# Kernel optimization log

Hardware: AMD Instinct MI355X
Metric: run time of the kernel (lower is better)

## Reference

```python
import jax, jax.numpy as jnp
import numpy as np

Q, L = 512, 4096


def setup_inputs() -> dict:
    key = jax.random.key(0)
    ks = jax.random.split(key, 12)
    def rn(k, shape, s=0.05):
        return jax.random.normal(k, shape, jnp.float32) * s
    return {
        "reactions": jax.random.normal(ks[0], (1, Q, 256), jnp.float32),
        "protein":   jax.random.normal(ks[1], (1, L, 1024), jnp.float32),
        # conv1d(1024->256, k=1) == pointwise linear
        "Wc":  rn(ks[2], (256, 1024)), "bc":  jnp.zeros((256,), jnp.float32),
        "W1":  rn(ks[3], (64, 256)),   "b1":  jnp.zeros((64,), jnp.float32),
        "W2":  rn(ks[4], (64, 256)),   "b2":  jnp.zeros((64,), jnp.float32),
        "Wa":  rn(ks[5], (64, 64)),    "ba":  jnp.zeros((64,), jnp.float32),
        "Wpa": rn(ks[6], (64, 64)),    "bpa": jnp.zeros((64,), jnp.float32),
        "Wra": rn(ks[7], (64, 64)),    "bra": jnp.zeros((64,), jnp.float32),
        "Wf1": rn(ks[8], (256, 128)),  "bf1": jnp.zeros((256,), jnp.float32),
        "Wf2": rn(ks[9], (128, 256)),  "bf2": jnp.zeros((128,), jnp.float32),
        "Wf3": rn(ks[10], (1, 128)),   "bf3": jnp.zeros((1,), jnp.float32),
    }


def reference(reactions, protein, Wc, bc, W1, b1, W2, b2, Wa, ba,
              Wpa, bpa, Wra, bra, Wf1, bf1, Wf2, bf2, Wf3, bf3):
    # protein: [1, L, 1024] -> 1x1 conv over channels == linear -> [L, 256]
    p = jax.nn.relu(protein[0] @ Wc.T + bc)
    # reactions: [1, Q, 256] -> [Q, 64]
    r = jax.nn.relu(reactions[0] @ W2.T + b2)
    # protein tokens -> [L, 64]
    k = jax.nn.relu(p @ W1.T + b1)

    ra = r @ Wra.T + bra            # [Q, 64]
    pa = k @ Wpa.T + bpa            # [L, 64]
    # broadcast outer-sum + relu + small linear: [Q, L, 64]
    A = jax.nn.relu(ra[:, None, :] + pa[None, :, :]) @ Wa.T + ba

    r_gate = jax.nn.sigmoid(jnp.mean(A, axis=1))   # [Q, 64]
    p_gate = jax.nn.sigmoid(jnp.mean(A, axis=0))   # [L, 64]

    rxnfp = r + r * r_gate                          # [Q, 64]
    prot = jnp.max(k + k * p_gate, axis=0)          # [64]  maxpool over L

    ctx = jnp.concatenate(
        [rxnfp, jnp.broadcast_to(prot, (rxnfp.shape[0], 64))], axis=1)  # [Q,128]

    # dropout layers are identity in eval mode
    h = jax.nn.leaky_relu(ctx @ Wf1.T + bf1)
    h = jax.nn.leaky_relu(h @ Wf2.T + bf2)
    out = h @ Wf3.T + bf3
    return out.reshape(-1)                          # [Q]
```

## Files before the change

### kernel.cpp

```cpp
#include <hip/hip_runtime.h>
#include <math.h>

#define TPB 256

typedef __attribute__((ext_vector_type(8))) short s16x8;
typedef __attribute__((ext_vector_type(4))) float f32x4;

constexpr unsigned OFF_P    = 0u;
constexpr unsigned OFF_K    = OFF_P    + 4096u*256u;
constexpr unsigned OFF_PA   = OFF_K    + 4096u*64u;
constexpr unsigned OFF_R    = OFF_PA   + 4096u*64u;
constexpr unsigned OFF_RA   = OFF_R    + 512u*64u;
constexpr unsigned OFF_SRP  = OFF_RA   + 512u*64u;
constexpr unsigned OFF_PMAX = OFF_SRP  + 8u*512u*64u;
constexpr unsigned OFF_W1T  = OFF_PMAX + 256u*64u;
constexpr unsigned OFF_W2T  = OFF_W1T  + 256u*64u;
constexpr unsigned OFF_WF1T = OFF_W2T  + 256u*64u;
constexpr unsigned OFF_WF2T = OFF_WF1T + 128u*256u;

__device__ __forceinline__ short f2bf(float x) {
  union { float f; unsigned u; } v; v.f = x;
  unsigned r = v.u + 0x7FFFu + ((v.u >> 16) & 1u);
  return (short)(r >> 16);
}

__global__ __launch_bounds__(TPB, 2) void k1_gemm(
    const float* __restrict__ prot, const float* __restrict__ Wc,
    const float* __restrict__ bc,   const float* __restrict__ W1,
    const float* __restrict__ W2,   const float* __restrict__ Wf1,
    const float* __restrict__ Wf2,  float* __restrict__ ws)
{
  int bid = blockIdx.x;
  int tid = threadIdx.x;
  if (bid >= 128) {
    int tb = bid - 128;
    if (tb < 2) {
      const float* W = (tb == 0) ? W1 : W2;
      float* WT = ws + ((tb == 0) ? OFF_W1T : OFF_W2T);
      for (int it = 0; it < 64; ++it) {
        int idx = it * TPB + tid;
        WT[idx] = W[(idx & 63) * 256 + (idx >> 6)];
      }
    } else if (tb < 4) {
      int h = tb - 2;
      for (int it = 0; it < 64; ++it) {
        int idx = h * 16384 + it * TPB + tid;
        ws[OFF_WF1T + idx] = Wf1[(idx & 255) * 128 + (idx >> 8)];
      }
    } else {
      int h = tb - 4;
      for (int it = 0; it < 64; ++it) {
        int idx = h * 16384 + it * TPB + tid;
        ws[OFF_WF2T + idx] = Wf2[(idx & 127) * 256 + (idx >> 7)];
      }
    }
    return;
  }

  __shared__ __align__(16) short Asm[64 * 72];
  __shared__ __align__(16) short Bsm[128 * 72];

  int m0 = (bid >> 1) * 64;
  int n0 = (bid & 1) * 128;
  int wave = tid >> 6, lane = tid & 63;
  int wm = (wave >> 1) * 32, wn = (wave & 1) * 64;
  int lm = lane & 15, quad = lane >> 4;

  int arow = tid >> 2, aseg = (tid & 3) * 16;
  int brow = tid >> 1, bseg = (tid & 1) * 32;

  const float* Ag = prot + (size_t)(m0 + arow) * 1024 + aseg;
  const float* Bg = Wc   + (size_t)(n0 + brow) * 1024 + bseg;

  float4 a4[4], b4[8];
#pragma unroll
  for (int i = 0; i < 4; ++i) a4[i] = *(const float4*)(Ag + i * 4);
#pragma unroll
  for (int i = 0; i < 8; ++i) b4[i] = *(const float4*)(Bg + i * 4);

  f32x4 acc[2][4] = {};

  for (int kc = 0; kc < 16; ++kc) {
    __syncthreads();
    {
      s16x8 s0, s1;
      s0[0]=f2bf(a4[0].x); s0[1]=f2bf(a4[0].y); s0[2]=f2bf(a4[0].z); s0[3]=f2bf(a4[0].w);
      s0[4]=f2bf(a4[1].x); s0[5]=f2bf(a4[1].y); s0[6]=f2bf(a4[1].z); s0[7]=f2bf(a4[1].w);
      s1[0]=f2bf(a4[2].x); s1[1]=f2bf(a4[2].y); s1[2]=f2bf(a4[2].z); s1[3]=f2bf(a4[2].w);
      s1[4]=f2bf(a4[3].x); s1[5]=f2bf(a4[3].y); s1[6]=f2bf(a4[3].z); s1[7]=f2bf(a4[3].w);
      *(s16x8*)&Asm[arow * 72 + aseg]     = s0;
      *(s16x8*)&Asm[arow * 72 + aseg + 8] = s1;
    }
#pragma unroll
    for (int h = 0; h < 4; ++h) {
      s16x8 s;
      s[0]=f2bf(b4[h*2].x);   s[1]=f2bf(b4[h*2].y);
      s[2]=f2bf(b4[h*2].z);   s[3]=f2bf(b4[h*2].w);
      s[4]=f2bf(b4[h*2+1].x); s[5]=f2bf(b4[h*2+1].y);
      s[6]=f2bf(b4[h*2+1].z); s[7]=f2bf(b4[h*2+1].w);
      *(s16x8*)&Bsm[brow * 72 + bseg + h * 8] = s;
    }
    if (kc < 15) {
#pragma unroll
      for (int i = 0; i < 4; ++i) a4[i] = *(const float4*)(Ag + (kc + 1) * 64 + i * 4);
#pragma unroll
      for (int i = 0; i < 8; ++i) b4[i] = *(const float4*)(Bg + (kc + 1) * 64 + i * 4);
    }
    __syncthreads();
#pragma unroll
    for (int ks = 0; ks < 2; ++ks) {
      s16x8 af[2], bfv[4];
#pragma unroll
      for (int mi = 0; mi < 2; ++mi)
        af[mi] = *(const s16x8*)&Asm[(wm + mi * 16 + lm) * 72 + ks * 32 + quad * 8];
#pragma unroll
      for (int ni = 0; ni < 4; ++ni)
        bfv[ni] = *(const s16x8*)&Bsm[(wn + ni * 16 + lm) * 72 + ks * 32 + quad * 8];
#pragma unroll
      for (int mi = 0; mi < 2; ++mi)
#pragma unroll
        for (int ni = 0; ni < 4; ++ni)
          acc[mi][ni] = __builtin_amdgcn_mfma_f32_16x16x32_bf16(
              af[mi], bfv[ni], acc[mi][ni], 0, 0, 0);
    }
  }

#pragma unroll
  for (int ni = 0; ni < 4; ++ni) {
    int col = n0 + wn + ni * 16 + lm;
    float bcv = bc[col];
#pragma unroll
    for (int mi = 0; mi < 2; ++mi) {
#pragma unroll
      for (int r = 0; r < 4; ++r) {
        int row = m0 + wm + mi * 16 + quad * 4 + r;
        ws[OFF_P + (unsigned)row * 256u + col] = fmaxf(acc[mi][ni][r] + bcv, 0.f);
      }
    }
  }
}

__global__ __launch_bounds__(TPB) void k2_heads(
    const float* __restrict__ reactions,
    const float* __restrict__ b1,  const float* __restrict__ b2,
    const float* __restrict__ Wpa, const float* __restrict__ bpa,
    const float* __restrict__ Wra, const float* __restrict__ bra,
    float* __restrict__ ws)
{
  __shared__ float ps[16 * 256];
  __shared__ float ks_[16 * 65];
  __shared__ float wst[64 * 65];
  int bid = blockIdx.x, tid = threadIdx.x;
  bool isProt = bid < 256;
  int row0 = (isProt ? bid : (bid - 256)) * 16;
  const float* src  = isProt ? (ws + OFF_P) : reactions;
  const float* WTg  = ws + (isProt ? OFF_W1T : OFF_W2T);
  const float* bv   = isProt ? b1 : b2;
  const float* W2nd = isProt ? Wpa : Wra;
  const float* b2nd = isProt ? bpa : bra;
  float* out1 = ws + (isProt ? OFF_K : OFF_R);
  float* out2 = ws + (isProt ? OFF_PA : OFF_RA);

#pragma unroll
  for (int it = 0; it < 4; ++it) {
    int i4 = it * TPB + tid;
    int row = i4 >> 6, c4 = (i4 & 63) * 4;
    *(float4*)&ps[row * 256 + c4] =
        *(const float4*)(src + (row0 + row) * 256u + c4);
  }
#pragma unroll
  for (int it = 0; it < 16; ++it) {
    int idx = it * TPB + tid;
    int a = idx >> 6, b = idx & 63;
    wst[b * 65 + a] = W2nd[idx];
  }
  __syncthreads();

  int j = tid & 63, g = tid >> 6;
  float acc[4];
  float bb = bv[j];
#pragma unroll
  for (int i = 0; i < 4; ++i) acc[i] = bb;
#pragma unroll 8
  for (int cc = 0; cc < 256; ++cc) {
    float w = WTg[cc * 64 + j];
#pragma unroll
    for (int i = 0; i < 4; ++i)
      acc[i] += ps[(g * 4 + i) * 256 + cc] * w;
  }
#pragma unroll
  for (int i = 0; i < 4; ++i) {
    float kv = fmaxf(acc[i], 0.f);
    int row = g * 4 + i;
    out1[(row0 + row) * 64u + j] = kv;
    ks_[row * 65 + j] = kv;
  }
  __syncthreads();

  float bb2 = b2nd[j];
  float acc2[4];
#pragma unroll
  for (int i = 0; i < 4; ++i) acc2[i] = bb2;
#pragma unroll 8
  for (int jj = 0; jj < 64; ++jj) {
    float w = wst[jj * 65 + j];
#pragma unroll
    for (int i = 0; i < 4; ++i)
      acc2[i] += ks_[(g * 4 + i) * 65 + jj] * w;
  }
#pragma unroll
  for (int i = 0; i < 4; ++i)
    out2[(row0 + g * 4 + i) * 64u + j] = acc2[i];
}

__global__ __launch_bounds__(TPB) void k3_interact(
    const float* __restrict__ Wa, const float* __restrict__ ba,
    float* __restrict__ ws)
{
  __shared__ float sm[9536];
  int bid = blockIdx.x, tid = threadIdx.x;
  int c = tid & 63, g = tid >> 6;
  const float* ra = ws + OFF_RA;
  const float* pa = ws + OFF_PA;

  if (bid < 256) {
    int qt = bid >> 3, ls = bid & 7;
    int q0 = qt * 16, l0 = ls * 512;
    float u[4], acc[4];
#pragma unroll
    for (int i = 0; i < 4; ++i) {
      u[i] = ra[(q0 + g * 4 + i) * 64u + c];
      acc[i] = 0.f;
    }
    for (int chunk = 0; chunk < 8; ++chunk) {
      unsigned base = (unsigned)(l0 + chunk * 64) * 64u;
      for (int it = 0; it < 4; ++it) {
        int i4 = it * TPB + tid;
        int row = i4 >> 4, c4 = (i4 & 15) * 4;
        *(float4*)&sm[row * 64 + c4] = *(const float4*)(pa + base + row * 64 + c4);
      }
      __syncthreads();
#pragma unroll 4
      for (int ll = 0; ll < 64; ++ll) {
        float x = sm[ll * 64 + c];
#pragma unroll
        for (int i = 0; i < 4; ++i) acc[i] += fmaxf(u[i] + x, 0.f);
      }
      __syncthreads();
    }
#pragma unroll
    for (int i = 0; i < 4; ++i)
      ws[OFF_SRP + (unsigned)(ls * 512 + q0 + g * 4 + i) * 64u + c] = acc[i];
  } else {
    int b = bid - 256;
    int l0 = b * 16;
    for (int it = 0; it < 16; ++it) {
      int idx = it * TPB + tid;
      int a = idx >> 6, bb = idx & 63;
      sm[5120 + bb * 65 + a] = Wa[idx];
    }
    float v[4], acc[4];
#pragma unroll
    for (int i = 0; i < 4; ++i) {
      v[i] = pa[(unsigned)(l0 + g * 4 + i) * 64u + c];
      acc[i] = 0.f;
    }
    for (int chunk = 0; chunk < 8; ++chunk) {
      unsigned base = (unsigned)(chunk * 64) * 64u;
      for (int it = 0; it < 4; ++it) {
        int i4 = it * TPB + tid;
        int row = i4 >> 4, c4 = (i4 & 15) * 4;
        *(float4*)&sm[row * 64 + c4] = *(const float4*)(ra + base + row * 64 + c4);
      }
      __syncthreads();
#pragma unroll 4
      for (int qq = 0; qq < 64; ++qq) {
        float x = sm[qq * 64 + c];
#pragma unroll
        for (int i = 0; i < 4; ++i) acc[i] += fmaxf(v[i] + x, 0.f);
      }
      __syncthreads();
    }
#pragma unroll
    for (int i = 0; i < 4; ++i) sm[4096 + (g * 4 + i) * 64 + c] = acc[i];
    __syncthreads();
    float vmax = 0.f;
    float bac = ba[c];
#pragma unroll
    for (int i = 0; i < 4; ++i) {
      int ll = g * 4 + i;
      float dot = 0.f;
#pragma unroll 8
      for (int jj = 0; jj < 64; ++jj)
        dot += sm[4096 + ll * 64 + jj] * sm[5120 + jj * 65 + c];
      float pg = 1.f / (1.f + __expf(-(dot * (1.f / 512.f) + bac)));
      float val = ws[OFF_K + (unsigned)(l0 + ll) * 64u + c] * (1.f + pg);
      vmax = fmaxf(vmax, val);
    }
    sm[9280 + g * 64 + c] = vmax;
    __syncthreads();
    if (tid < 64) {
      float m = fmaxf(fmaxf(sm[9280 + tid], sm[9280 + 64 + tid]),
                      fmaxf(sm[9280 + 128 + tid], sm[9280 + 192 + tid]));
      ws[OFF_PMAX + (unsigned)b * 64u + tid] = m;
    }
  }
}

__global__ __launch_bounds__(TPB) void k4_final(
    const float* __restrict__ Wa,  const float* __restrict__ ba,
    const float* __restrict__ bf1, const float* __restrict__ bf2,
    const float* __restrict__ Wf3, const float* __restrict__ bf3,
    const float* __restrict__ ws,  float* __restrict__ out)
{
  __shared__ float wa[64 * 65];
  __shared__ float mr[256];
  __shared__ float pm[256];
  __shared__ float prot[64];
  __shared__ float rx[256];
  __shared__ float h1s[4 * 256];
  __shared__ float h2s[4 * 128];
  int bid = blockIdx.x, tid = threadIdx.x;
  int q0 = bid * 4;
  int q = tid >> 6, c = tid & 63;

  for (int it = 0; it < 16; ++it) {
    int idx = it * TPB + tid;
    wa[(idx >> 6) * 65 + (idx & 63)] = Wa[idx];
  }
  {
    float s = 0.f;
#pragma unroll
    for (int ls = 0; ls < 8; ++ls)
      s += ws[OFF_SRP + (unsigned)(ls * 512 + q0 + q) * 64u + c];
    mr[q * 64 + c] = s * (1.f / 4096.f);
  }
  {
    float m = 0.f;
    for (int i = 0; i < 64; ++i)
      m = fmaxf(m, ws[OFF_PMAX + (unsigned)(q * 64 + i) * 64u + c]);
    pm[q * 64 + c] = m;
  }
  __syncthreads();
  if (tid < 64)
    prot[tid] = fmaxf(fmaxf(pm[tid], pm[64 + tid]),
                      fmaxf(pm[128 + tid], pm[192 + tid]));
  __syncthreads();
  {
    float dot = 0.f;
#pragma unroll 8
    for (int j = 0; j < 64; ++j)
      dot += mr[q * 64 + j] * wa[c * 65 + j];
    float g = 1.f / (1.f + __expf(-(dot + ba[c])));
    rx[q * 64 + c] = ws[OFF_R + (unsigned)(q0 + q) * 64u + c] * (1.f + g);
  }
  __syncthreads();
  {
    int n = tid;
    const float* wf1t = ws + OFF_WF1T;
    float a0 = 0, a1 = 0, a2 = 0, a3 = 0, c1 = 0;
#pragma unroll 4
    for (int j = 0; j < 64; ++j) {
      float w1 = wf1t[j * 256 + n];
      float w2 = wf1t[(64 + j) * 256 + n];
      c1 += prot[j] * w2;
      a0 += rx[j] * w1;
      a1 += rx[64 + j] * w1;
      a2 += rx[128 + j] * w1;
      a3 += rx[192 + j] * w1;
    }
    float bb = bf1[n] + c1;
    float v;
    v = a0 + bb; h1s[0 * 256 + n] = v > 0.f ? v : 0.01f * v;
    v = a1 + bb; h1s[1 * 256 + n] = v > 0.f ? v : 0.01f * v;
    v = a2 + bb; h1s[2 * 256 + n] = v > 0.f ? v : 0.01f * v;
    v = a3 + bb; h1s[3 * 256 + n] = v > 0.f ? v : 0.01f * v;
  }
  __syncthreads();
  {
    int m = tid & 127, qh = tid >> 7;
    const float* wf2t = ws + OFF_WF2T;
    const float* h1a = h1s + (qh * 2) * 256;
    const float* h1b = h1s + (qh * 2 + 1) * 256;
    float b0 = 0, b1 = 0;
#pragma unroll 4
    for (int j = 0; j < 256; ++j) {
      float w = wf2t[j * 128 + m];
      b0 += h1a[j] * w;
      b1 += h1b[j] * w;
    }
    float bb = bf2[m];
    float v0 = b0 + bb, v1 = b1 + bb;
    h2s[(qh * 2) * 128 + m]     = v0 > 0.f ? v0 : 0.01f * v0;
    h2s[(qh * 2 + 1) * 128 + m] = v1 > 0.f ? v1 : 0.01f * v1;
  }
  __syncthreads();
  {
    float v = h2s[q * 128 + c] * Wf3[c] + h2s[q * 128 + 64 + c] * Wf3[64 + c];
#pragma unroll
    for (int off = 32; off > 0; off >>= 1) v += __shfl_down(v, off);
    if (c == 0) out[q0 + q] = v + bf3[0];
  }
}

extern "C" void kernel_launch(void* const* d_in, const int* in_sizes, int n_in,
                              void* d_out, int out_size, void* d_ws, size_t ws_size,
                              hipStream_t stream)
{
  const float* reactions = (const float*)d_in[0];
  const float* protein   = (const float*)d_in[1];
  const float* Wc  = (const float*)d_in[2];
  const float* bc  = (const float*)d_in[3];
  const float* W1  = (const float*)d_in[4];
  const float* b1  = (const float*)d_in[5];
  const float* W2  = (const float*)d_in[6];
  const float* b2  = (const float*)d_in[7];
  const float* Wa  = (const float*)d_in[8];
  const float* ba  = (const float*)d_in[9];
  const float* Wpa = (const float*)d_in[10];
  const float* bpa = (const float*)d_in[11];
  const float* Wra = (const float*)d_in[12];
  const float* bra = (const float*)d_in[13];
  const float* Wf1 = (const float*)d_in[14];
  const float* bf1 = (const float*)d_in[15];
  const float* Wf2 = (const float*)d_in[16];
  const float* bf2 = (const float*)d_in[17];
  const float* Wf3 = (const float*)d_in[18];
  const float* bf3 = (const float*)d_in[19];
  float* ws  = (float*)d_ws;
  float* out = (float*)d_out;

  hipLaunchKernelGGL(k1_gemm, dim3(134), dim3(TPB), 0, stream,
                     protein, Wc, bc, W1, W2, Wf1, Wf2, ws);
  hipLaunchKernelGGL(k2_heads, dim3(288), dim3(TPB), 0, stream,
                     reactions, b1, b2, Wpa, bpa, Wra, bra, ws);
  hipLaunchKernelGGL(k3_interact, dim3(512), dim3(TPB), 0, stream,
                     Wa, ba, ws);
  hipLaunchKernelGGL(k4_final, dim3(128), dim3(TPB), 0, stream,
                     Wa, ba, bf1, bf2, Wf3, bf3, ws, out);
}
```

Measured before the change: 205.3 us.

## Use MFMA bf16 in head kernel, tiled weight transposes, packed bf16 conversion

The head kernel now runs both of its small projections (256->64 and 64->64) as bf16 MFMA tiles with operands staged in shared memory, instead of scalar fp32 FMAs over pre-transposed weights. As a result the W1/W2 transposes drop out of the first kernel, and the Wf1/Wf2 transposes become coalesced 32x32 shared-memory tile transposes spread across 8 blocks. Float-to-bf16 conversion uses the packed intrinsic in place of manual per-element rounding. The final kernel handles 2 queries per block across 256 blocks to spread the MLP tail over more CUs. Dropping the head projections to bf16 lowers their precision.

```diff
diff --git a/kernel.cpp b/kernel.cpp
--- a/kernel.cpp
+++ b/kernel.cpp
@@ -1,4 +1,5 @@
 #include <hip/hip_runtime.h>
+#include <hip/hip_bf16.h>
 #include <math.h>
 
 #define TPB 256
@@ -23,36 +24,48 @@
   unsigned r = v.u + 0x7FFFu + ((v.u >> 16) & 1u);
   return (short)(r >> 16);
 }
+__device__ __forceinline__ unsigned pkbf(float a, float b) {
+  __hip_bfloat162 h = __float22bfloat162_rn(make_float2(a, b));
+  union { __hip_bfloat162 h2; unsigned u; } v; v.h2 = h;
+  return v.u;
+}
+union U8 { s16x8 s; unsigned u[4]; };
 
 __global__ __launch_bounds__(TPB, 2) void k1_gemm(
     const float* __restrict__ prot, const float* __restrict__ Wc,
-    const float* __restrict__ bc,   const float* __restrict__ W1,
-    const float* __restrict__ W2,   const float* __restrict__ Wf1,
+    const float* __restrict__ bc,   const float* __restrict__ Wf1,
     const float* __restrict__ Wf2,  float* __restrict__ ws)
 {
   int bid = blockIdx.x;
   int tid = threadIdx.x;
   if (bid >= 128) {
+    __shared__ float tl[32 * 33];
     int tb = bid - 128;
-    if (tb < 2) {
-      const float* W = (tb == 0) ? W1 : W2;
-      float* WT = ws + ((tb == 0) ? OFF_W1T : OFF_W2T);
-      for (int it = 0; it < 64; ++it) {
+    for (int i = 0; i < 8; ++i) {
+      int t = tb * 8 + i;
+      const float* S; float* D; int snc, dnc, sr, sc;
+      if (t < 32) {
+        S = Wf1; D = ws + OFF_WF1T; snc = 128; dnc = 256;
+        sr = (t >> 2) * 32; sc = (t & 3) * 32;
+      } else {
+        int t2 = t - 32;
+        S = Wf2; D = ws + OFF_WF2T; snc = 256; dnc = 128;
+        sr = (t2 >> 3) * 32; sc = (t2 & 7) * 32;
+      }
+#pragma unroll
+      for (int it = 0; it < 4; ++it) {
         int idx = it * TPB + tid;
-        WT[idx] = W[(idx & 63) * 256 + (idx >> 6)];
-      }
-    } else if (tb < 4) {
-      int h = tb - 2;
-      for (int it = 0; it < 64; ++it) {
-        int idx = h * 16384 + it * TPB + tid;
-        ws[OFF_WF1T + idx] = Wf1[(idx & 255) * 128 + (idx >> 8)];
-      }
-    } else {
-      int h = tb - 4;
-      for (int it = 0; it < 64; ++it) {
-        int idx = h * 16384 + it * TPB + tid;
-        ws[OFF_WF2T + idx] = Wf2[(idx & 127) * 256 + (idx >> 7)];
-      }
+        int r = idx >> 5, c = idx & 31;
+        tl[c * 33 + r] = S[(size_t)(sr + r) * snc + sc + c];
+      }
+      __syncthreads();
+#pragma unroll
+      for (int it = 0; it < 4; ++it) {
+        int idx = it * TPB + tid;
+        int r = idx >> 5, c = idx & 31;
+        D[(size_t)(sc + r) * dnc + sr + c] = tl[r * 33 + c];
+      }
+      __syncthreads();
     }
     return;
   }
@@ -83,22 +96,22 @@
   for (int kc = 0; kc < 16; ++kc) {
     __syncthreads();
     {
-      s16x8 s0, s1;
-      s0[0]=f2bf(a4[0].x); s0[1]=f2bf(a4[0].y); s0[2]=f2bf(a4[0].z); s0[3]=f2bf(a4[0].w);
-      s0[4]=f2bf(a4[1].x); s0[5]=f2bf(a4[1].y); s0[6]=f2bf(a4[1].z); s0[7]=f2bf(a4[1].w);
-      s1[0]=f2bf(a4[2].x); s1[1]=f2bf(a4[2].y); s1[2]=f2bf(a4[2].z); s1[3]=f2bf(a4[2].w);
-      s1[4]=f2bf(a4[3].x); s1[5]=f2bf(a4[3].y); s1[6]=f2bf(a4[3].z); s1[7]=f2bf(a4[3].w);
-      *(s16x8*)&Asm[arow * 72 + aseg]     = s0;
-      *(s16x8*)&Asm[arow * 72 + aseg + 8] = s1;
+      U8 s0, s1;
+      s0.u[0] = pkbf(a4[0].x, a4[0].y); s0.u[1] = pkbf(a4[0].z, a4[0].w);
+      s0.u[2] = pkbf(a4[1].x, a4[1].y); s0.u[3] = pkbf(a4[1].z, a4[1].w);
+      s1.u[0] = pkbf(a4[2].x, a4[2].y); s1.u[1] = pkbf(a4[2].z, a4[2].w);
+      s1.u[2] = pkbf(a4[3].x, a4[3].y); s1.u[3] = pkbf(a4[3].z, a4[3].w);
+      *(s16x8*)&Asm[arow * 72 + aseg]     = s0.s;
+      *(s16x8*)&Asm[arow * 72 + aseg + 8] = s1.s;
     }
 #pragma unroll
     for (int h = 0; h < 4; ++h) {
-      s16x8 s;
-      s[0]=f2bf(b4[h*2].x);   s[1]=f2bf(b4[h*2].y);
-      s[2]=f2bf(b4[h*2].z);   s[3]=f2bf(b4[h*2].w);
-      s[4]=f2bf(b4[h*2+1].x); s[5]=f2bf(b4[h*2+1].y);
-      s[6]=f2bf(b4[h*2+1].z); s[7]=f2bf(b4[h*2+1].w);
-      *(s16x8*)&Bsm[brow * 72 + bseg + h * 8] = s;
+      U8 s;
+      s.u[0] = pkbf(b4[h*2].x,   b4[h*2].y);
+      s.u[1] = pkbf(b4[h*2].z,   b4[h*2].w);
+      s.u[2] = pkbf(b4[h*2+1].x, b4[h*2+1].y);
+      s.u[3] = pkbf(b4[h*2+1].z, b4[h*2+1].w);
+      *(s16x8*)&Bsm[brow * 72 + bseg + h * 8] = s.s;
     }
     if (kc < 15) {
 #pragma unroll
@@ -140,77 +153,121 @@
   }
 }
 
-__global__ __launch_bounds__(TPB) void k2_heads(
+__global__ __launch_bounds__(TPB, 2) void k2_heads(
     const float* __restrict__ reactions,
-    const float* __restrict__ b1,  const float* __restrict__ b2,
+    const float* __restrict__ W1,  const float* __restrict__ b1,
+    const float* __restrict__ W2,  const float* __restrict__ b2,
     const float* __restrict__ Wpa, const float* __restrict__ bpa,
     const float* __restrict__ Wra, const float* __restrict__ bra,
     float* __restrict__ ws)
 {
-  __shared__ float ps[16 * 256];
-  __shared__ float ks_[16 * 65];
-  __shared__ float wst[64 * 65];
+  __shared__ __align__(16) short Asm[32 * 264];
+  __shared__ __align__(16) short Bsm[64 * 264];
+  __shared__ __align__(16) short Ksm[32 * 72];
+  __shared__ __align__(16) short Wsm[64 * 72];
   int bid = blockIdx.x, tid = threadIdx.x;
-  bool isProt = bid < 256;
-  int row0 = (isProt ? bid : (bid - 256)) * 16;
+  bool isProt = bid < 128;
+  int row0 = (isProt ? bid : (bid - 128)) * 32;
   const float* src  = isProt ? (ws + OFF_P) : reactions;
-  const float* WTg  = ws + (isProt ? OFF_W1T : OFF_W2T);
+  const float* Wst1 = isProt ? W1 : W2;
   const float* bv   = isProt ? b1 : b2;
-  const float* W2nd = isProt ? Wpa : Wra;
+  const float* Wst2 = isProt ? Wpa : Wra;
   const float* b2nd = isProt ? bpa : bra;
   float* out1 = ws + (isProt ? OFF_K : OFF_R);
   float* out2 = ws + (isProt ? OFF_PA : OFF_RA);
 
-#pragma unroll
-  for (int it = 0; it < 4; ++it) {
-    int i4 = it * TPB + tid;
-    int row = i4 >> 6, c4 = (i4 & 63) * 4;
-    *(float4*)&ps[row * 256 + c4] =
-        *(const float4*)(src + (row0 + row) * 256u + c4);
-  }
-#pragma unroll
-  for (int it = 0; it < 16; ++it) {
-    int idx = it * TPB + tid;
-    int a = idx >> 6, b = idx & 63;
-    wst[b * 65 + a] = W2nd[idx];
-  }
-  __syncthreads();
-
-  int j = tid & 63, g = tid >> 6;
-  float acc[4];
-  float bb = bv[j];
-#pragma unroll
-  for (int i = 0; i < 4; ++i) acc[i] = bb;
-#pragma unroll 8
-  for (int cc = 0; cc < 256; ++cc) {
-    float w = WTg[cc * 64 + j];
-#pragma unroll
-    for (int i = 0; i < 4; ++i)
-      acc[i] += ps[(g * 4 + i) * 256 + cc] * w;
-  }
-#pragma unroll
-  for (int i = 0; i < 4; ++i) {
-    float kv = fmaxf(acc[i], 0.f);
-    int row = g * 4 + i;
-    out1[(row0 + row) * 64u + j] = kv;
-    ks_[row * 65 + j] = kv;
-  }
-  __syncthreads();
-
-  float bb2 = b2nd[j];
-  float acc2[4];
-#pragma unroll
-  for (int i = 0; i < 4; ++i) acc2[i] = bb2;
-#pragma unroll 8
-  for (int jj = 0; jj < 64; ++jj) {
-    float w = wst[jj * 65 + j];
-#pragma unroll
-    for (int i = 0; i < 4; ++i)
-      acc2[i] += ks_[(g * 4 + i) * 65 + jj] * w;
-  }
-#pragma unroll
-  for (int i = 0; i < 4; ++i)
-    out2[(row0 + g * 4 + i) * 64u + j] = acc2[i];
+  {
+    int row = tid >> 3, seg = (tid & 7) * 32;
+    const float* sp = src + (size_t)(row0 + row) * 256 + seg;
+    float4 f[8];
+#pragma unroll
+    for (int i = 0; i < 8; ++i) f[i] = *(const float4*)(sp + i * 4);
+#pragma unroll
+    for (int i = 0; i < 4; ++i) {
+      U8 s;
+      s.u[0] = pkbf(f[2*i].x,   f[2*i].y);
+      s.u[1] = pkbf(f[2*i].z,   f[2*i].w);
+      s.u[2] = pkbf(f[2*i+1].x, f[2*i+1].y);
+      s.u[3] = pkbf(f[2*i+1].z, f[2*i+1].w);
+      *(s16x8*)&Asm[row * 264 + seg + i * 8] = s.s;
+    }
+  }
+  {
+    int row = tid >> 2, seg = (tid & 3) * 64;
+    const float* sp = Wst1 + (size_t)row * 256 + seg;
+#pragma unroll
+    for (int i = 0; i < 8; ++i) {
+      float4 fa = *(const float4*)(sp + i * 8);
+      float4 fb = *(const float4*)(sp + i * 8 + 4);
+      U8 s;
+      s.u[0] = pkbf(fa.x, fa.y); s.u[1] = pkbf(fa.z, fa.w);
+      s.u[2] = pkbf(fb.x, fb.y); s.u[3] = pkbf(fb.z, fb.w);
+      *(s16x8*)&Bsm[row * 264 + seg + i * 8] = s.s;
+    }
+  }
+  {
+    int row = tid >> 2, seg = (tid & 3) * 16;
+    const float* sp = Wst2 + (size_t)row * 64 + seg;
+#pragma unroll
+    for (int i = 0; i < 2; ++i) {
+      float4 fa = *(const float4*)(sp + i * 8);
+      float4 fb = *(const float4*)(sp + i * 8 + 4);
+      U8 s;
+      s.u[0] = pkbf(fa.x, fa.y); s.u[1] = pkbf(fa.z, fa.w);
+      s.u[2] = pkbf(fb.x, fb.y); s.u[3] = pkbf(fb.z, fb.w);
+      *(s16x8*)&Wsm[row * 72 + seg + i * 8] = s.s;
+    }
+  }
+  __syncthreads();
+
+  int wave = tid >> 6, lane = tid & 63;
+  int lm = lane & 15, quad = lane >> 4;
+  int wm = (wave >> 1) * 16, wn = (wave & 1) * 32;
+
+  f32x4 acc[2] = {};
+#pragma unroll
+  for (int kc = 0; kc < 8; ++kc) {
+    s16x8 a = *(const s16x8*)&Asm[(wm + lm) * 264 + kc * 32 + quad * 8];
+#pragma unroll
+    for (int ni = 0; ni < 2; ++ni) {
+      s16x8 b = *(const s16x8*)&Bsm[(wn + ni * 16 + lm) * 264 + kc * 32 + quad * 8];
+      acc[ni] = __builtin_amdgcn_mfma_f32_16x16x32_bf16(a, b, acc[ni], 0, 0, 0);
+    }
+  }
+#pragma unroll
+  for (int ni = 0; ni < 2; ++ni) {
+    int col = wn + ni * 16 + lm;
+    float bb = bv[col];
+#pragma unroll
+    for (int r = 0; r < 4; ++r) {
+      int row = wm + quad * 4 + r;
+      float kv = fmaxf(acc[ni][r] + bb, 0.f);
+      out1[(size_t)(row0 + row) * 64 + col] = kv;
+      Ksm[row * 72 + col] = f2bf(kv);
+    }
+  }
+  __syncthreads();
+
+  f32x4 acc2[2] = {};
+#pragma unroll
+  for (int kc = 0; kc < 2; ++kc) {
+    s16x8 a = *(const s16x8*)&Ksm[(wm + lm) * 72 + kc * 32 + quad * 8];
+#pragma unroll
+    for (int ni = 0; ni < 2; ++ni) {
+      s16x8 b = *(const s16x8*)&Wsm[(wn + ni * 16 + lm) * 72 + kc * 32 + quad * 8];
+      acc2[ni] = __builtin_amdgcn_mfma_f32_16x16x32_bf16(a, b, acc2[ni], 0, 0, 0);
+    }
+  }
+#pragma unroll
+  for (int ni = 0; ni < 2; ++ni) {
+    int col = wn + ni * 16 + lm;
+    float bb = b2nd[col];
+#pragma unroll
+    for (int r = 0; r < 4; ++r) {
+      int row = wm + quad * 4 + r;
+      out2[(size_t)(row0 + row) * 64 + col] = acc2[ni][r] + bb;
+    }
+  }
 }
 
 __global__ __launch_bounds__(TPB) void k3_interact(
@@ -314,93 +371,91 @@
     const float* __restrict__ ws,  float* __restrict__ out)
 {
   __shared__ float wa[64 * 65];
-  __shared__ float mr[256];
+  __shared__ float mr[128];
   __shared__ float pm[256];
   __shared__ float prot[64];
-  __shared__ float rx[256];
-  __shared__ float h1s[4 * 256];
-  __shared__ float h2s[4 * 128];
+  __shared__ float rx[128];
+  __shared__ float h1s[2 * 256];
+  __shared__ float h2s[2 * 128];
+  __shared__ float red[8];
   int bid = blockIdx.x, tid = threadIdx.x;
-  int q0 = bid * 4;
-  int q = tid >> 6, c = tid & 63;
+  int q0 = bid * 2;
 
   for (int it = 0; it < 16; ++it) {
     int idx = it * TPB + tid;
     wa[(idx >> 6) * 65 + (idx & 63)] = Wa[idx];
   }
-  {
+  if (tid < 128) {
+    int q = tid >> 6, c = tid & 63;
     float s = 0.f;
 #pragma unroll
     for (int ls = 0; ls < 8; ++ls)
       s += ws[OFF_SRP + (unsigned)(ls * 512 + q0 + q) * 64u + c];
-    mr[q * 64 + c] = s * (1.f / 4096.f);
-  }
-  {
+    mr[tid] = s * (1.f / 4096.f);
+  }
+  {
+    int c = tid & 63, ch = tid >> 6;
     float m = 0.f;
+#pragma unroll 8
     for (int i = 0; i < 64; ++i)
-      m = fmaxf(m, ws[OFF_PMAX + (unsigned)(q * 64 + i) * 64u + c]);
-    pm[q * 64 + c] = m;
+      m = fmaxf(m, ws[OFF_PMAX + (unsigned)(ch * 64 + i) * 64u + c]);
+    pm[ch * 64 + c] = m;
   }
   __syncthreads();
   if (tid < 64)
     prot[tid] = fmaxf(fmaxf(pm[tid], pm[64 + tid]),
                       fmaxf(pm[128 + tid], pm[192 + tid]));
   __syncthreads();
-  {
+  if (tid < 128) {
+    int q = tid >> 6, c = tid & 63;
     float dot = 0.f;
 #pragma unroll 8
     for (int j = 0; j < 64; ++j)
       dot += mr[q * 64 + j] * wa[c * 65 + j];
     float g = 1.f / (1.f + __expf(-(dot + ba[c])));
-    rx[q * 64 + c] = ws[OFF_R + (unsigned)(q0 + q) * 64u + c] * (1.f + g);
+    rx[tid] = ws[OFF_R + (unsigned)(q0 + q) * 64u + c] * (1.f + g);
   }
   __syncthreads();
   {
     int n = tid;
     const float* wf1t = ws + OFF_WF1T;
-    float a0 = 0, a1 = 0, a2 = 0, a3 = 0, c1 = 0;
-#pragma unroll 4
+    float a0 = 0, a1 = 0, c1 = 0;
+#pragma unroll 8
     for (int j = 0; j < 64; ++j) {
       float w1 = wf1t[j * 256 + n];
       float w2 = wf1t[(64 + j) * 256 + n];
       c1 += prot[j] * w2;
       a0 += rx[j] * w1;
       a1 += rx[64 + j] * w1;
-      a2 += rx[128 + j] * w1;
-      a3 += rx[192 + j] * w1;
     }
     float bb = bf1[n] + c1;
     float v;
-    v = a0 + bb; h1s[0 * 256 + n] = v > 0.f ? v : 0.01f * v;
-    v = a1 + bb; h1s[1 * 256 + n] = v > 0.f ? v : 0.01f * v;
-    v = a2 + bb; h1s[2 * 256 + n] = v > 0.f ? v : 0.01f * v;
-    v = a3 + bb; h1s[3 * 256 + n] = v > 0.f ? v : 0.01f * v;
+    v = a0 + bb; h1s[n]       = v > 0.f ? v : 0.01f * v;
+    v = a1 + bb; h1s[256 + n] = v > 0.f ? v : 0.01f * v;
   }
   __syncthreads();
   {
     int m = tid & 127, qh = tid >> 7;
     const float* wf2t = ws + OFF_WF2T;
-    const float* h1a = h1s + (qh * 2) * 256;
-    const float* h1b = h1s + (qh * 2 + 1) * 256;
-    float b0 = 0, b1 = 0;
-#pragma unroll 4
-    for (int j = 0; j < 256; ++j) {
-      float w = wf2t[j * 128 + m];
-      b0 += h1a[j] * w;
-      b1 += h1b[j] * w;
-    }
-    float bb = bf2[m];
-    float v0 = b0 + bb, v1 = b1 + bb;
-    h2s[(qh * 2) * 128 + m]     = v0 > 0.f ? v0 : 0.01f * v0;
-    h2s[(qh * 2 + 1) * 128 + m] = v1 > 0.f ? v1 : 0.01f * v1;
-  }
-  __syncthreads();
-  {
-    float v = h2s[q * 128 + c] * Wf3[c] + h2s[q * 128 + 64 + c] * Wf3[64 + c];
+    const float* h1a = h1s + qh * 256;
+    float b0 = 0;
+#pragma unroll 8
+    for (int j = 0; j < 256; ++j)
+      b0 += h1a[j] * wf2t[j * 128 + m];
+    float v = b0 + bf2[m];
+    h2s[qh * 128 + m] = v > 0.f ? v : 0.01f * v;
+  }
+  __syncthreads();
+  {
+    int wave = tid >> 6, lane = tid & 63;
+    int q = wave >> 1, h = wave & 1;
+    float v = h2s[q * 128 + h * 64 + lane] * Wf3[h * 64 + lane];
 #pragma unroll
     for (int off = 32; off > 0; off >>= 1) v += __shfl_down(v, off);
-    if (c == 0) out[q0 + q] = v + bf3[0];
-  }
+    if (lane == 0) red[wave] = v;
+  }
+  __syncthreads();
+  if (tid < 2) out[q0 + tid] = red[tid * 2] + red[tid * 2 + 1] + bf3[0];
 }
 
 extern "C" void kernel_launch(void* const* d_in, const int* in_sizes, int n_in,
@@ -430,12 +485,12 @@
   float* ws  = (float*)d_ws;
   float* out = (float*)d_out;
 
-  hipLaunchKernelGGL(k1_gemm, dim3(134), dim3(TPB), 0, stream,
-                     protein, Wc, bc, W1, W2, Wf1, Wf2, ws);
-  hipLaunchKernelGGL(k2_heads, dim3(288), dim3(TPB), 0, stream,
-                     reactions, b1, b2, Wpa, bpa, Wra, bra, ws);
+  hipLaunchKernelGGL(k1_gemm, dim3(136), dim3(TPB), 0, stream,
+                     protein, Wc, bc, Wf1, Wf2, ws);
+  hipLaunchKernelGGL(k2_heads, dim3(144), dim3(TPB), 0, stream,
+                     reactions, W1, b1, W2, b2, Wpa, bpa, Wra, bra, ws);
   hipLaunchKernelGGL(k3_interact, dim3(512), dim3(TPB), 0, stream,
                      Wa, ba, ws);
-  hipLaunchKernelGGL(k4_final, dim3(128), dim3(TPB), 0, stream,
+  hipLaunchKernelGGL(k4_final, dim3(256), dim3(TPB), 0, stream,
                      Wa, ba, bf1, bf2, Wf3, bf3, ws, out);
 }
```

Result: faster. 190.3 us (-7.3%).
